# Optimization experiments

Measured on AMD Instinct MI355X. Metric: run time of the kernel, lower is better.

Reference implementation:

```python
import jax, jax.numpy as jnp
import numpy as np

EPS = 1e-12

def _dot(x, y):
    return jnp.sum(x * y, axis=-1)

def _safe(x):
    # avoid div-by-zero for degenerate triangles / unused where-branches
    return jnp.where(jnp.abs(x) < EPS, EPS, x)

def _closest_point_on_tri(p, a, b, c):
    """Ericson real-time-collision-detection closest point on triangle.
    p: [B,Q,1,3]; a,b,c: [B,1,F,3]. Returns [B,Q,F,3]."""
    ab = b - a
    ac = c - a
    ap = p - a
    d1 = _dot(ab, ap)
    d2 = _dot(ac, ap)
    bp = p - b
    d3 = _dot(ab, bp)
    d4 = _dot(ac, bp)
    cp = p - c
    d5 = _dot(ab, cp)
    d6 = _dot(ac, cp)
    vc = d1 * d4 - d3 * d2
    vb = d5 * d2 - d1 * d6
    va = d3 * d6 - d5 * d4
    # candidate points (all computed densely, selected by masks)
    t_ab = (d1 / _safe(d1 - d3))[..., None]
    t_ac = (d2 / _safe(d2 - d6))[..., None]
    t_bc = ((d4 - d3) / _safe((d4 - d3) + (d5 - d6)))[..., None]
    denom = _safe(va + vb + vc)
    v = (vb / denom)[..., None]
    w = (vc / denom)[..., None]
    res = a + ab * v + ac * w  # face interior
    cond_bc = ((va <= 0) & ((d4 - d3) >= 0) & ((d5 - d6) >= 0))[..., None]
    cond_ac = ((vb <= 0) & (d2 >= 0) & (d6 <= 0))[..., None]
    cond_c = ((d6 >= 0) & (d5 <= d6))[..., None]
    cond_ab = ((vc <= 0) & (d1 >= 0) & (d3 <= 0))[..., None]
    cond_b = ((d3 >= 0) & (d4 <= d3))[..., None]
    cond_a = ((d1 <= 0) & (d2 <= 0))[..., None]
    res = jnp.where(cond_bc, b + (c - b) * t_bc, res)
    res = jnp.where(cond_ac, a + ac * t_ac, res)
    res = jnp.where(cond_c, c, res)
    res = jnp.where(cond_ab, a + ab * t_ab, res)
    res = jnp.where(cond_b, b, res)
    res = jnp.where(cond_a, a, res)
    return res

def setup_inputs() -> dict:
    key = jax.random.key(0)
    k1, k2, k3 = jax.random.split(key, 3)
    B, nQ, nV, nF = 1, 8192, 1024, 2048
    vertices = jax.random.normal(k1, (B, nV, 3), dtype=jnp.float32)
    query = jax.random.normal(k2, (B, nQ, 3), dtype=jnp.float32)
    faces = jax.random.randint(k3, (nF, 3), 0, nV, dtype=jnp.int32)
    return {"faces": faces, "vertices": vertices, "query": query}

def reference(faces, vertices, query):
    # gather triangle vertices: [B, F, 3(verts), 3(xyz)]
    tri = vertices[:, faces, :]
    a = tri[:, :, 0][:, None]  # [B,1,F,3]
    b = tri[:, :, 1][:, None]
    c = tri[:, :, 2][:, None]
    p = query[:, :, None, :]   # [B,Q,1,3]
    cp = _closest_point_on_tri(p, a, b, c)        # [B,Q,F,3]
    d2 = jnp.sum((p - cp) ** 2, axis=-1)          # [B,Q,F]
    idx = jnp.argmin(d2, axis=-1)                 # [B,Q]
    B_, Q_ = idx.shape
    cp_best = jnp.take_along_axis(
        cp, jnp.broadcast_to(idx[:, :, None, None], (B_, Q_, 1, 3)), axis=2
    )[:, :, 0]                                    # [B,Q,3]
    d2_best = jnp.take_along_axis(d2, idx[:, :, None], axis=2)[:, :, 0]
    # face normals for sign (outside if along normal), per-face then gathered
    n = jnp.cross(tri[:, :, 1] - tri[:, :, 0], tri[:, :, 2] - tri[:, :, 0])  # [B,F,3]
    n_best = jnp.take_along_axis(n, jnp.broadcast_to(idx[:, :, None], (B_, Q_, 3)) % n.shape[1] * 0 + idx[:, :, None], axis=1)  # [B,Q,3]
    sign = jnp.where(jnp.sum((query - cp_best) * n_best, axis=-1) >= 0, 1.0, -1.0)
    sdist = sign * jnp.sqrt(jnp.maximum(d2_best, 0.0))
    phi = jnp.concatenate([cp_best, sdist[..., None]], axis=-1)  # [B,Q,4]
    return phi
```

## Files before the change

kernel.cpp:

```cpp
#include <hip/hip_runtime.h>
#include <stdint.h>


#define QPB 256
#define FC  32
#define RECF 20

__device__ __forceinline__ float safe32(float x) {
    return (fabsf(x) < 1e-12f) ? 1e-12f : x;
}

__device__ __forceinline__ float cp32(
    float px, float py, float pz, const float* __restrict__ t,
    float& rx, float& ry, float& rz)
{
#pragma clang fp contract(off)
    float ax  = t[0],  ay  = t[1],  az  = t[2];
    float bx  = t[3],  by  = t[4],  bz  = t[5];
    float cx  = t[6],  cy  = t[7],  cz  = t[8];
    float abx = t[9],  aby = t[10], abz = t[11];
    float acx = t[12], acy = t[13], acz = t[14];
    float cbx = t[15], cby = t[16], cbz = t[17];

    float apx = px - ax, apy = py - ay, apz = pz - az;
    float bpx = px - bx, bpy = py - by, bpz = pz - bz;
    float qpx = px - cx, qpy = py - cy, qpz = pz - cz;

    float d1 = ((abx * apx) + (aby * apy)) + (abz * apz);
    float d2 = ((acx * apx) + (acy * apy)) + (acz * apz);
    float d3 = ((abx * bpx) + (aby * bpy)) + (abz * bpz);
    float d4 = ((acx * bpx) + (acy * bpy)) + (acz * bpz);
    float d5 = ((abx * qpx) + (aby * qpy)) + (abz * qpz);
    float d6 = ((acx * qpx) + (acy * qpy)) + (acz * qpz);

    float vc = (d1 * d4) - (d3 * d2);
    float vb = (d5 * d2) - (d1 * d6);
    float va = (d3 * d6) - (d5 * d4);
    float e1 = d4 - d3;
    float e2 = d5 - d6;

    bool ca  = (d1 <= 0.0f) && (d2 <= 0.0f);
    bool cb_ = (d3 >= 0.0f) && (d4 <= d3);
    bool cab = (vc <= 0.0f) && (d1 >= 0.0f) && (d3 <= 0.0f);
    bool cc  = (d6 >= 0.0f) && (d5 <= d6);
    bool cac = (vb <= 0.0f) && (d2 >= 0.0f) && (d6 <= 0.0f);
    bool cbc = (va <= 0.0f) && (e1 >= 0.0f) && (e2 >= 0.0f);

    bool tk  = ca;
    bool m_b  = cb_ && !tk;  tk = tk || cb_;
    bool m_ab = cab && !tk;  tk = tk || cab;
    bool m_c  = cc  && !tk;  tk = tk || cc;
    bool m_ac = cac && !tk;  tk = tk || cac;
    bool m_bc = cbc && !tk;  tk = tk || cbc;
    bool m_in = !tk;

    float denom_raw = (va + vb) + vc;
    float num1 = m_ab ? d1 : m_ac ? d2 : m_bc ? e1 : m_in ? vb : 0.0f;
    float den1_raw = m_ab ? (d1 - d3) : m_ac ? (d2 - d6)
                   : m_bc ? (e1 + e2) : m_in ? denom_raw : 1.0f;
    float den1  = safe32(den1_raw);
    float denom = safe32(denom_raw);
    float num2  = m_in ? vc : 0.0f;
    float q1 = num1 / den1;
    float q2 = num2 / denom;

    bool sel_b = m_b || m_bc;
    float basx = m_c ? cx : sel_b ? bx : ax;
    float basy = m_c ? cy : sel_b ? by : ay;
    float basz = m_c ? cz : sel_b ? bz : az;

    bool s_ab = m_ab || m_in;
    float t1x = m_bc ? cbx : m_ac ? acx : s_ab ? abx : 0.0f;
    float t1y = m_bc ? cby : m_ac ? acy : s_ab ? aby : 0.0f;
    float t1z = m_bc ? cbz : m_ac ? acz : s_ab ? abz : 0.0f;

    float t2x = m_in ? acx : 0.0f;
    float t2y = m_in ? acy : 0.0f;
    float t2z = m_in ? acz : 0.0f;

    rx = (basx + (t1x * q1)) + (t2x * q2);
    ry = (basy + (t1y * q1)) + (t2y * q2);
    rz = (basz + (t1z * q1)) + (t2z * q2);

    float dx = px - rx, dy = py - ry, dz = pz - rz;
    return ((dx * dx) + (dy * dy)) + (dz * dz);
}

__global__ void k_prep(const int* __restrict__ faces, const float* __restrict__ verts,
                       float* __restrict__ tris, unsigned long long* __restrict__ keys,
                       int nF, int nQ)
{
#pragma clang fp contract(off)
    int i = blockIdx.x * 256 + threadIdx.x;
    if (i < nQ) keys[i] = 0xffffffffffffffffULL;
    if (i < nF) {
        int i0 = faces[i * 3 + 0], i1 = faces[i * 3 + 1], i2 = faces[i * 3 + 2];
        float ax = verts[i0 * 3], ay = verts[i0 * 3 + 1], az = verts[i0 * 3 + 2];
        float bx = verts[i1 * 3], by = verts[i1 * 3 + 1], bz = verts[i1 * 3 + 2];
        float cx = verts[i2 * 3], cy = verts[i2 * 3 + 1], cz = verts[i2 * 3 + 2];
        float* t = &tris[i * RECF];
        t[0]  = ax; t[1]  = ay; t[2]  = az; t[3]  = bx;
        t[4]  = by; t[5]  = bz; t[6]  = cx; t[7]  = cy;
        t[8]  = cz;
        t[9]  = bx - ax; t[10] = by - ay; t[11] = bz - az;
        t[12] = cx - ax; t[13] = cy - ay; t[14] = cz - az;
        t[15] = cx - bx; t[16] = cy - by; t[17] = cz - bz;
        t[18] = 0.0f; t[19] = 0.0f;
    }
}

__global__ __launch_bounds__(QPB) void k_main(
    const float* __restrict__ tris, const float* __restrict__ query,
    unsigned long long* __restrict__ keys, int nF, int nQ)
{
    const int fbase = blockIdx.y * FC;
    const int nf = min(FC, nF - fbase);

    const int q = blockIdx.x * QPB + threadIdx.x;
    if (q >= nQ) return;
    const float px = query[q * 3], py = query[q * 3 + 1], pz = query[q * 3 + 2];

    float best = 3.402823466e38f;
    int bidx = 0x7fffffff;
#pragma unroll 2
    for (int f = 0; f < nf; ++f) {
        float rx, ry, rz;
        float d2 = cp32(px, py, pz, &tris[(size_t)(fbase + f) * RECF],
                        rx, ry, rz);
        if (d2 < best) { best = d2; bidx = fbase + f; }
    }
    unsigned long long key =
        ((unsigned long long)__float_as_uint(best) << 32) | (unsigned)bidx;
    atomicMin(&keys[q], key);
}

__global__ void k_final(const float* __restrict__ tris, const float* __restrict__ query,
                        const unsigned long long* __restrict__ keys,
                        float* __restrict__ out, int nQ)
{
#pragma clang fp contract(off)
    int q = blockIdx.x * 256 + threadIdx.x;
    if (q >= nQ) return;
    unsigned long long key = keys[q];
    unsigned idx = (unsigned)(key & 0xffffffffu);
    float best_d2 = __uint_as_float((unsigned)(key >> 32));

    const float px = query[q * 3], py = query[q * 3 + 1], pz = query[q * 3 + 2];
    const float* t = &tris[(size_t)idx * RECF];
    float rx, ry, rz;
    cp32(px, py, pz, t, rx, ry, rz);

    float abx = t[9],  aby = t[10], abz = t[11];
    float acx = t[12], acy = t[13], acz = t[14];
    float nx = (aby * acz) - (abz * acy);
    float ny = (abz * acx) - (abx * acz);
    float nz = (abx * acy) - (aby * acx);

    float dx = px - rx, dy = py - ry, dz = pz - rz;
    float sdot = ((dx * nx) + (dy * ny)) + (dz * nz);
    float sgn = (sdot >= 0.0f) ? 1.0f : -1.0f;
    float sdist = sgn * __fsqrt_rn(fmaxf(best_d2, 0.0f));

    out[q * 4 + 0] = rx;
    out[q * 4 + 1] = ry;
    out[q * 4 + 2] = rz;
    out[q * 4 + 3] = sdist;
}

extern "C" void kernel_launch(void* const* d_in, const int* in_sizes, int n_in,
                              void* d_out, int out_size, void* d_ws, size_t ws_size,
                              hipStream_t stream) {
    const int* faces = (const int*)d_in[0];
    const float* verts = (const float*)d_in[1];
    const float* query = (const float*)d_in[2];
    float* out = (float*)d_out;

    const int nF = in_sizes[0] / 3;
    const int nQ = in_sizes[2] / 3;

    unsigned long long* keys = (unsigned long long*)d_ws;
    float* tris = (float*)((char*)d_ws + (size_t)nQ * 8);

    int prep_threads = (nQ > nF ? nQ : nF);
    k_prep<<<(prep_threads + 255) / 256, 256, 0, stream>>>(faces, verts, tris, keys, nF, nQ);

    dim3 grid((nQ + QPB - 1) / QPB, (nF + FC - 1) / FC);
    k_main<<<grid, QPB, 0, stream>>>(tris, query, keys, nF, nQ);

    k_final<<<(nQ + 255) / 256, 256, 0, stream>>>(tris, query, keys, out, nQ);
}
```

Measured before the change: 126.6 us.

## Scan faces with algebraic squared distance and recheck ambiguous queries exactly

Faces are precomputed into an extended record of dot products, squared norms, normals and reciprocal edge lengths. Distances can then be written in closed form from a few dot products with the query, with no need to build the closest point. Each wave now handles one query across all faces, staged through shared memory in chunks. It tracks the best and second-best distance instead of using a grid of atomicMin calls. Queries whose top two candidates fall within a margin are rescanned with the exact reference-order arithmetic, which trades extra work and rounding risk for a cheaper main scan.

```diff
diff --git a/kernel.cpp b/kernel.cpp
--- a/kernel.cpp
+++ b/kernel.cpp
@@ -2,9 +2,9 @@
 #include <stdint.h>
 
 
-#define QPB 256
-#define FC  32
-#define RECF 20
+#define RECA 20
+#define RECB 28
+#define CHUNK 256
 
 __device__ __forceinline__ float safe32(float x) {
     return (fabsf(x) < 1e-12f) ? 1e-12f : x;
@@ -42,14 +42,14 @@
     bool ca  = (d1 <= 0.0f) && (d2 <= 0.0f);
     bool cb_ = (d3 >= 0.0f) && (d4 <= d3);
     bool cab = (vc <= 0.0f) && (d1 >= 0.0f) && (d3 <= 0.0f);
-    bool cc  = (d6 >= 0.0f) && (d5 <= d6);
+    bool cc_ = (d6 >= 0.0f) && (d5 <= d6);
     bool cac = (vb <= 0.0f) && (d2 >= 0.0f) && (d6 <= 0.0f);
     bool cbc = (va <= 0.0f) && (e1 >= 0.0f) && (e2 >= 0.0f);
 
     bool tk  = ca;
     bool m_b  = cb_ && !tk;  tk = tk || cb_;
     bool m_ab = cab && !tk;  tk = tk || cab;
-    bool m_c  = cc  && !tk;  tk = tk || cc;
+    bool m_c  = cc_ && !tk;  tk = tk || cc_;
     bool m_ac = cac && !tk;  tk = tk || cac;
     bool m_bc = cbc && !tk;  tk = tk || cbc;
     bool m_in = !tk;
@@ -86,69 +86,14 @@
     return ((dx * dx) + (dy * dy)) + (dz * dz);
 }
 
-__global__ void k_prep(const int* __restrict__ faces, const float* __restrict__ verts,
-                       float* __restrict__ tris, unsigned long long* __restrict__ keys,
-                       int nF, int nQ)
+__device__ __forceinline__ void write_result(
+    int q, int widx, const float* __restrict__ trisA,
+    float px, float py, float pz, float* __restrict__ out)
 {
 #pragma clang fp contract(off)
-    int i = blockIdx.x * 256 + threadIdx.x;
-    if (i < nQ) keys[i] = 0xffffffffffffffffULL;
-    if (i < nF) {
-        int i0 = faces[i * 3 + 0], i1 = faces[i * 3 + 1], i2 = faces[i * 3 + 2];
-        float ax = verts[i0 * 3], ay = verts[i0 * 3 + 1], az = verts[i0 * 3 + 2];
-        float bx = verts[i1 * 3], by = verts[i1 * 3 + 1], bz = verts[i1 * 3 + 2];
-        float cx = verts[i2 * 3], cy = verts[i2 * 3 + 1], cz = verts[i2 * 3 + 2];
-        float* t = &tris[i * RECF];
-        t[0]  = ax; t[1]  = ay; t[2]  = az; t[3]  = bx;
-        t[4]  = by; t[5]  = bz; t[6]  = cx; t[7]  = cy;
-        t[8]  = cz;
-        t[9]  = bx - ax; t[10] = by - ay; t[11] = bz - az;
-        t[12] = cx - ax; t[13] = cy - ay; t[14] = cz - az;
-        t[15] = cx - bx; t[16] = cy - by; t[17] = cz - bz;
-        t[18] = 0.0f; t[19] = 0.0f;
-    }
-}
-
-__global__ __launch_bounds__(QPB) void k_main(
-    const float* __restrict__ tris, const float* __restrict__ query,
-    unsigned long long* __restrict__ keys, int nF, int nQ)
-{
-    const int fbase = blockIdx.y * FC;
-    const int nf = min(FC, nF - fbase);
-
-    const int q = blockIdx.x * QPB + threadIdx.x;
-    if (q >= nQ) return;
-    const float px = query[q * 3], py = query[q * 3 + 1], pz = query[q * 3 + 2];
-
-    float best = 3.402823466e38f;
-    int bidx = 0x7fffffff;
-#pragma unroll 2
-    for (int f = 0; f < nf; ++f) {
-        float rx, ry, rz;
-        float d2 = cp32(px, py, pz, &tris[(size_t)(fbase + f) * RECF],
-                        rx, ry, rz);
-        if (d2 < best) { best = d2; bidx = fbase + f; }
-    }
-    unsigned long long key =
-        ((unsigned long long)__float_as_uint(best) << 32) | (unsigned)bidx;
-    atomicMin(&keys[q], key);
-}
-
-__global__ void k_final(const float* __restrict__ tris, const float* __restrict__ query,
-                        const unsigned long long* __restrict__ keys,
-                        float* __restrict__ out, int nQ)
-{
-#pragma clang fp contract(off)
-    int q = blockIdx.x * 256 + threadIdx.x;
-    if (q >= nQ) return;
-    unsigned long long key = keys[q];
-    unsigned idx = (unsigned)(key & 0xffffffffu);
-    float best_d2 = __uint_as_float((unsigned)(key >> 32));
-
-    const float px = query[q * 3], py = query[q * 3 + 1], pz = query[q * 3 + 2];
-    const float* t = &tris[(size_t)idx * RECF];
+    const float* t = &trisA[(size_t)widx * RECA];
     float rx, ry, rz;
-    cp32(px, py, pz, t, rx, ry, rz);
+    float best_d2 = cp32(px, py, pz, t, rx, ry, rz);
 
     float abx = t[9],  aby = t[10], abz = t[11];
     float acx = t[12], acy = t[13], acz = t[14];
@@ -165,6 +110,199 @@
     out[q * 4 + 1] = ry;
     out[q * 4 + 2] = rz;
     out[q * 4 + 3] = sdist;
+}
+
+__global__ void k_prep(const int* __restrict__ faces, const float* __restrict__ verts,
+                       float* __restrict__ trisA, float* __restrict__ trisB, int nF)
+{
+#pragma clang fp contract(off)
+    int i = blockIdx.x * 256 + threadIdx.x;
+    if (i >= nF) return;
+    int i0 = faces[i * 3 + 0], i1 = faces[i * 3 + 1], i2 = faces[i * 3 + 2];
+    float ax = verts[i0 * 3], ay = verts[i0 * 3 + 1], az = verts[i0 * 3 + 2];
+    float bx = verts[i1 * 3], by = verts[i1 * 3 + 1], bz = verts[i1 * 3 + 2];
+    float cx = verts[i2 * 3], cy = verts[i2 * 3 + 1], cz = verts[i2 * 3 + 2];
+
+    float abx = bx - ax, aby = by - ay, abz = bz - az;
+    float acx = cx - ax, acy = cy - ay, acz = cz - az;
+    float cbx = cx - bx, cby = cy - by, cbz = cz - bz;
+
+    float* t = &trisA[(size_t)i * RECA];
+    t[0]  = ax; t[1]  = ay; t[2]  = az; t[3]  = bx;
+    t[4]  = by; t[5]  = bz; t[6]  = cx; t[7]  = cy;
+    t[8]  = cz;
+    t[9]  = abx; t[10] = aby; t[11] = abz;
+    t[12] = acx; t[13] = acy; t[14] = acz;
+    t[15] = cbx; t[16] = cby; t[17] = cbz;
+    t[18] = 0.0f; t[19] = 0.0f;
+
+    float aba = abx * ax + aby * ay + abz * az;
+    float abb = abx * bx + aby * by + abz * bz;
+    float abc = abx * cx + aby * cy + abz * cz;
+    float aca = acx * ax + acy * ay + acz * az;
+    float acb = acx * bx + acy * by + acz * bz;
+    float acc = acx * cx + acy * cy + acz * cz;
+    float aa = ax * ax + ay * ay + az * az;
+    float bb = bx * bx + by * by + bz * bz;
+    float ccv = cx * cx + cy * cy + cz * cz;
+    float nx = aby * acz - abz * acy;
+    float ny = abz * acx - abx * acz;
+    float nz = abx * acy - aby * acx;
+    float na = nx * ax + ny * ay + nz * az;
+    float abab = abx * abx + aby * aby + abz * abz;
+    float acac = acx * acx + acy * acy + acz * acz;
+    float cbcb = cbx * cbx + cby * cby + cbz * cbz;
+    float nn   = nx * nx + ny * ny + nz * nz;
+
+    float* u = &trisB[(size_t)i * RECB];
+    u[0]  = abx; u[1]  = aby; u[2]  = abz; u[3]  = acx;
+    u[4]  = acy; u[5]  = acz; u[6]  = aba; u[7]  = abb;
+    u[8]  = abc; u[9]  = aca; u[10] = acb; u[11] = acc;
+    u[12] = aa;  u[13] = bb;  u[14] = ccv; u[15] = ax;
+    u[16] = ay;  u[17] = az;  u[18] = nx;  u[19] = ny;
+    u[20] = nz;  u[21] = na;  u[22] = 1.0f / safe32(abab);
+    u[23] = 1.0f / safe32(acac);
+    u[24] = 1.0f / safe32(cbcb);
+    u[25] = 1.0f / safe32(nn);
+    u[26] = 0.0f; u[27] = 0.0f;
+}
+
+__global__ __launch_bounds__(256) void k_scan(
+    const float* __restrict__ trisB, const float* __restrict__ query,
+    int* __restrict__ widx, int* __restrict__ wamb, int nF, int nQ)
+{
+    __shared__ float4 sB[CHUNK * (RECB / 4)];
+    const int tid = threadIdx.x;
+    const int lane = tid & 63;
+    const int q = blockIdx.x * 4 + (tid >> 6);
+    const bool valid = q < nQ;
+
+    float px = 0.f, py = 0.f, pz = 0.f, pp = 0.f;
+    if (valid) {
+        px = query[q * 3]; py = query[q * 3 + 1]; pz = query[q * 3 + 2];
+        pp = px * px + py * py + pz * pz;
+    }
+
+    float m1 = 3.402823466e38f, m2 = 3.402823466e38f;
+    int i1 = 0x7fffffff;
+
+    const int nchunks = (nF + CHUNK - 1) / CHUNK;
+    for (int c = 0; c < nchunks; ++c) {
+        const int fbase = c * CHUNK;
+        const int cnt = min(CHUNK, nF - fbase);
+        __syncthreads();
+        {
+            const float4* src = (const float4*)&trisB[(size_t)fbase * RECB];
+            for (int i = tid; i < cnt * (RECB / 4); i += 256) sB[i] = src[i];
+        }
+        __syncthreads();
+        if (!valid) continue;
+
+#pragma unroll
+        for (int it = 0; it < CHUNK / 64; ++it) {
+            int j = it * 64 + lane;
+            if (j >= cnt) break;
+            int f = fbase + j;
+            const float4* r = &sB[j * (RECB / 4)];
+            float4 r0 = r[0], r1 = r[1], r2 = r[2], r3 = r[3];
+            float4 r4 = r[4], r5 = r[5], r6 = r[6];
+            float abx = r0.x, aby = r0.y, abz = r0.z, acx = r0.w;
+            float acy = r1.x, acz = r1.y, aba = r1.z, abb = r1.w;
+            float abc = r2.x, aca = r2.y, acb = r2.z, acc = r2.w;
+            float aa = r3.x, bb = r3.y, cc2 = r3.z, ax = r3.w;
+            float ay = r4.x, az = r4.y, nx = r4.z, ny = r4.w;
+            float nz = r5.x, na = r5.y, iab = r5.z, iac = r5.w;
+            float icb = r6.x, inn = r6.y;
+
+            float abp = abx * px + aby * py + abz * pz;
+            float acp = acx * px + acy * py + acz * pz;
+            float apd = ax * px + ay * py + az * pz;
+            float npd = nx * px + ny * py + nz * pz;
+            float d1 = abp - aba, d3 = abp - abb, d5 = abp - abc;
+            float d2 = acp - aca, d4 = acp - acb, d6 = acp - acc;
+            float vc = d1 * d4 - d3 * d2;
+            float vb = d5 * d2 - d1 * d6;
+            float va = d3 * d6 - d5 * d4;
+            float e1 = d4 - d3, e2 = d5 - d6;
+
+            float bpd = apd + abp, cpd = apd + acp;
+            float pap = (pp + aa) - 2.0f * apd;
+            float pbp = (pp + bb) - 2.0f * bpd;
+            float pcp = (pp + cc2) - 2.0f * cpd;
+            float nap = npd - na;
+
+            bool ca  = (d1 <= 0.0f) && (d2 <= 0.0f);
+            bool cb_ = (d3 >= 0.0f) && (d4 <= d3);
+            bool cab = (vc <= 0.0f) && (d1 >= 0.0f) && (d3 <= 0.0f);
+            bool cc_ = (d6 >= 0.0f) && (d5 <= d6);
+            bool cac = (vb <= 0.0f) && (d2 >= 0.0f) && (d6 <= 0.0f);
+            bool cbc = (va <= 0.0f) && (e1 >= 0.0f) && (e2 >= 0.0f);
+            bool tk  = ca;
+            bool m_b  = cb_ && !tk;  tk = tk || cb_;
+            bool m_ab = cab && !tk;  tk = tk || cab;
+            bool m_c  = cc_ && !tk;  tk = tk || cc_;
+            bool m_ac = cac && !tk;  tk = tk || cac;
+            bool m_bc = cbc && !tk;  tk = tk || cbc;
+            bool m_in = !tk;
+
+            float base = m_c ? pcp : (m_b || m_bc) ? pbp : pap;
+            float num  = m_ab ? d1 : m_ac ? d2 : m_bc ? e1 : nap;
+            float inv  = m_ab ? iab : m_ac ? iac : m_bc ? icb : inn;
+            bool corr_on = m_ab || m_ac || m_bc || m_in;
+            float tcorr = corr_on ? (num * num) * inv : 0.0f;
+            float d2a = m_in ? tcorr : (base - tcorr);
+
+            if (d2a < m1) { m2 = m1; m1 = d2a; i1 = f; }
+            else m2 = fminf(m2, d2a);
+        }
+    }
+
+    if (!valid) return;
+    for (int o = 32; o > 0; o >>= 1) {
+        float om1 = __shfl_down(m1, o);
+        int   oi1 = __shfl_down(i1, o);
+        float om2 = __shfl_down(m2, o);
+        float hi = fmaxf(m1, om1);
+        m2 = fminf(fminf(m2, om2), hi);
+        bool take = (om1 < m1) || (om1 == m1 && oi1 < i1);
+        if (take) { m1 = om1; i1 = oi1; }
+    }
+    if (lane == 0) {
+        float margin = 1e-3f * (1.0f + m1);
+        widx[q] = i1;
+        wamb[q] = (m2 <= m1 + margin) ? 1 : 0;
+    }
+}
+
+__global__ __launch_bounds__(256) void k_final(
+    const float* __restrict__ trisA, const float* __restrict__ query,
+    const int* __restrict__ widx, const int* __restrict__ wamb,
+    float* __restrict__ out, int nF, int nQ)
+{
+    const int q = blockIdx.x * 4 + (threadIdx.x >> 6);
+    const int lane = threadIdx.x & 63;
+    if (q >= nQ) return;
+
+    const float px = query[q * 3], py = query[q * 3 + 1], pz = query[q * 3 + 2];
+
+    if (!wamb[q]) {
+        if (lane == 0) write_result(q, widx[q], trisA, px, py, pz, out);
+        return;
+    }
+
+    float best = 3.402823466e38f;
+    int bidx = 0x7fffffff;
+    for (int f = lane; f < nF; f += 64) {
+        float rx, ry, rz;
+        float d2 = cp32(px, py, pz, &trisA[(size_t)f * RECA], rx, ry, rz);
+        if (d2 < best) { best = d2; bidx = f; }
+    }
+    for (int o = 32; o > 0; o >>= 1) {
+        float od = __shfl_down(best, o);
+        int   oi = __shfl_down(bidx, o);
+        if (od < best || (od == best && oi < bidx)) { best = od; bidx = oi; }
+    }
+    if (lane == 0) write_result(q, bidx, trisA, px, py, pz, out);
 }
 
 extern "C" void kernel_launch(void* const* d_in, const int* in_sizes, int n_in,
@@ -178,14 +316,15 @@
     const int nF = in_sizes[0] / 3;
     const int nQ = in_sizes[2] / 3;
 
-    unsigned long long* keys = (unsigned long long*)d_ws;
-    float* tris = (float*)((char*)d_ws + (size_t)nQ * 8);
-
-    int prep_threads = (nQ > nF ? nQ : nF);
-    k_prep<<<(prep_threads + 255) / 256, 256, 0, stream>>>(faces, verts, tris, keys, nF, nQ);
-
-    dim3 grid((nQ + QPB - 1) / QPB, (nF + FC - 1) / FC);
-    k_main<<<grid, QPB, 0, stream>>>(tris, query, keys, nF, nQ);
-
-    k_final<<<(nQ + 255) / 256, 256, 0, stream>>>(tris, query, keys, out, nQ);
-}
+    char* ws = (char*)d_ws;
+    float* trisA = (float*)ws;
+    float* trisB = (float*)(ws + (size_t)nF * RECA * 4);
+    int* widx = (int*)(ws + (size_t)nF * (RECA + RECB) * 4);
+    int* wamb = widx + nQ;
+
+    k_prep<<<(nF + 255) / 256, 256, 0, stream>>>(faces, verts, trisA, trisB, nF);
+
+    int qblocks = (nQ + 3) / 4;
+    k_scan<<<qblocks, 256, 0, stream>>>(trisB, query, widx, wamb, nF, nQ);
+    k_final<<<qblocks, 256, 0, stream>>>(trisA, query, widx, wamb, out, nF, nQ);
+}
```

New measurement: 190.3 us. +50.3%, slower.
